# Performance work log

Measured on AMD Instinct MI355X. Metric: run time of the kernel, lower is better.

Reference implementation:

```python
import jax, jax.numpy as jnp
import numpy as np

S, B, D = 2048, 2, 4096
H, KVH, HD = 32, 8, 128          # n_heads_q, n_kv_heads, head_dim
NREP = H // KVH                  # GQA repeat factor
ROPE_BASE = 10000.0


def _rope(x, cos, sin):
    # x: [B, S, h, HD]; cos/sin: [S, HD//2]
    xr = x.reshape(x.shape[:-1] + (-1, 2))
    x0, x1 = xr[..., 0], xr[..., 1]
    c = cos[None, :, None, :]
    s = sin[None, :, None, :]
    out = jnp.stack([x0 * c - x1 * s, x0 * s + x1 * c], axis=-1)
    return out.reshape(x.shape)


def setup_inputs() -> dict:
    key = jax.random.key(0)
    k0, k1, k2, k3, k4 = jax.random.split(key, 5)
    x = jax.random.normal(k0, (S, B, D), jnp.float32)
    inv_freq = 1.0 / (ROPE_BASE ** (np.arange(0, HD, 2, dtype=np.float64) / HD))  # [HD//2]
    t = np.arange(S, dtype=np.float64)[:, None] * inv_freq[None, :]               # [S, HD//2]
    freqs_cos = jnp.asarray(np.cos(t), jnp.float32)
    freqs_sin = jnp.asarray(np.sin(t), jnp.float32)
    scale = 0.02
    wq = jax.random.normal(k1, (H * HD, D), jnp.float32) * scale
    wk = jax.random.normal(k2, (KVH * HD, D), jnp.float32) * scale
    wv = jax.random.normal(k3, (KVH * HD, D), jnp.float32) * scale
    wo = jax.random.normal(k4, (D, H * HD), jnp.float32) * scale
    return {"x": x, "start_pos": 0, "freqs_cos": freqs_cos, "freqs_sin": freqs_sin,
            "wq": wq, "wk": wk, "wv": wv, "wo": wo}


def reference(x, start_pos, freqs_cos, freqs_sin, wq, wk, wv, wo):
    seq_len, batch, _ = x.shape
    # QKV projections (torch Linear: y = x @ W^T), then [S,B,*] -> [B,S,h,HD]
    q = (x @ wq.T).transpose(1, 0, 2).reshape(batch, seq_len, H, HD)
    k = (x @ wk.T).transpose(1, 0, 2).reshape(batch, seq_len, KVH, HD)
    v = (x @ wv.T).transpose(1, 0, 2).reshape(batch, seq_len, KVH, HD)
    # RoPE on q and k
    q = _rope(q, freqs_cos, freqs_sin)
    k = _rope(k, freqs_cos, freqs_sin)
    # repeat_kv (GQA)
    k = jnp.repeat(k, NREP, axis=2)
    v = jnp.repeat(v, NREP, axis=2)
    # [B, H, S, HD]
    q = q.transpose(0, 2, 1, 3)
    k = k.transpose(0, 2, 1, 3)
    v = v.transpose(0, 2, 1, 3)
    # causal scaled dot-product attention (SDPA is_causal=True equivalent)
    scores = jnp.einsum('bhqd,bhkd->bhqk', q, k) / np.float32(np.sqrt(HD))
    causal = jnp.tril(jnp.ones((seq_len, seq_len), dtype=bool))
    scores = jnp.where(causal[None, None], scores, jnp.float32(-jnp.inf))
    probs = jax.nn.softmax(scores.astype(jnp.float32), axis=-1).astype(q.dtype)
    out = jnp.einsum('bhqk,bhkd->bhqd', probs, v)
    # [B,H,S,HD] -> [B,S,H*HD] -> [S,B,H*HD]
    out = out.transpose(0, 2, 1, 3).reshape(batch, seq_len, H * HD).transpose(1, 0, 2)
    return out @ wo.T
```

## Files before the change

### kernel.cpp

```cpp
#include <hip/hip_runtime.h>

typedef __attribute__((ext_vector_type(8))) short s16x8;
typedef __attribute__((ext_vector_type(8))) __bf16 bf16x8;
typedef __attribute__((ext_vector_type(4))) float f32x4;

#define S_LEN 2048
#define KDIM  4096
#define CSOFT 0.12751743f

__device__ __forceinline__ unsigned short f2bf(float f) {
  unsigned u = __builtin_bit_cast(unsigned, f);
  u += 0x7fffu + ((u >> 16) & 1u);
  return (unsigned short)(u >> 16);
}

__device__ __forceinline__ f32x4 mfma_bf16(s16x8 a, s16x8 b, f32x4 c) {
  return __builtin_amdgcn_mfma_f32_16x16x32_bf16(
      __builtin_bit_cast(bf16x8, a), __builtin_bit_cast(bf16x8, b), c, 0, 0, 0);
}

__device__ __forceinline__ void gload_lds16(const unsigned short* g, void* l) {
  __builtin_amdgcn_global_load_lds(
      (const __attribute__((address_space(1))) void*)g,
      (__attribute__((address_space(3))) void*)l, 16, 0, 0);
}

__device__ __forceinline__ void cvt8(const float* p, unsigned short* out) {
  f32x4 a = *(const f32x4*)(p);
  f32x4 b = *(const f32x4*)(p + 4);
  s16x8 v;
  v[0] = (short)f2bf(a[0]); v[1] = (short)f2bf(a[1]);
  v[2] = (short)f2bf(a[2]); v[3] = (short)f2bf(a[3]);
  v[4] = (short)f2bf(b[0]); v[5] = (short)f2bf(b[1]);
  v[6] = (short)f2bf(b[2]); v[7] = (short)f2bf(b[3]);
  *(s16x8*)(out) = v;
}

__global__ void cvt_bf16(const float* __restrict__ in,
                         unsigned short* __restrict__ out, int n8) {
  int i = blockIdx.x * 256 + threadIdx.x;
  if (i >= n8) return;
  cvt8(in + (size_t)i * 8, out + (size_t)i * 8);
}

__global__ void cvt_all(const float* __restrict__ x, const float* __restrict__ wq,
                        const float* __restrict__ wk, const float* __restrict__ wv,
                        const float* __restrict__ wo,
                        unsigned short* __restrict__ ox, unsigned short* __restrict__ oq,
                        unsigned short* __restrict__ ok, unsigned short* __restrict__ ov,
                        unsigned short* __restrict__ oo) {
  int blk = blockIdx.x;
  const float* src;
  unsigned short* dst;
  int i;
  if (blk < 8192) { src = x; dst = ox; i = blk; }
  else if (blk < 16384) { src = wq; dst = oq; i = blk - 8192; }
  else if (blk < 18432) { src = wk; dst = ok; i = blk - 16384; }
  else if (blk < 20480) { src = wv; dst = ov; i = blk - 18432; }
  else { src = wo; dst = oo; i = blk - 20480; }
  size_t idx = ((size_t)i * 256 + threadIdx.x) * 8;
  cvt8(src + idx, dst + idx);
}

template <int EPI>
__global__ __launch_bounds__(512, 1)
void gemm256(const unsigned short* __restrict__ A,
             const unsigned short* __restrict__ B,
             void* __restrict__ Out,
             const float* __restrict__ cosT,
             const float* __restrict__ sinT) {
  const int K = KDIM;
  __shared__ __align__(16) unsigned short As[2 * 2 * 8192];
  __shared__ __align__(16) unsigned short Bs[2 * 2 * 8192];

  const int tid = threadIdx.x;
  const int lane = tid & 63, wid = tid >> 6;
  const int l15 = lane & 15, l4 = lane >> 4;
  const int wr = wid >> 2, wc = wid & 3;

  int bid = blockIdx.x;
  {
  }
  const int xcd = bid & 7, ii = bid >> 3;
  const int rt = (xcd >> 1) * 4 + (ii >> 3);
  const int ct = (xcd & 1) * 8 + (ii & 7);
  const int row0 = rt * 256, col0 = ct * 256;

  const int ch0 = tid, ch1 = 512 + tid;
  const int sr0 = ch0 >> 3, u0 = (ch0 & 7) ^ (sr0 & 7);
  const int sr1 = ch1 >> 3, u1 = (ch1 & 7) ^ (sr1 & 7);
  const unsigned short* A0p = A + (size_t)(row0 + sr0) * K + u0 * 8;
  const unsigned short* A1p = A + (size_t)(row0 + sr1) * K + u1 * 8;
  const unsigned short* B0p = B + (size_t)(col0 + sr0) * K + u0 * 8;
  const unsigned short* B1p = B + (size_t)(col0 + sr1) * K + u1 * 8;

  const int rdo0 = l15 * 128 + ((l4 ^ (l15 & 7)) << 4);
  const int rdo1 = l15 * 128 + (((4 | l4) ^ (l15 & 7)) << 4);

  f32x4 acc[8][4];
#pragma unroll
  for (int m = 0; m < 8; m++)
#pragma unroll
    for (int n = 0; n < 4; n++) acc[m][n] = f32x4{0.f, 0.f, 0.f, 0.f};

  auto stageA = [&](int buf, int h, int kt) {
    char* d = (char*)As + buf * 32768 + h * 16384 + wid * 1024;
    size_t so = (size_t)h * 128 * K + kt;
    gload_lds16(A0p + so, d);
    gload_lds16(A1p + so, d + 8192);
  };
  auto stageB = [&](int buf, int h, int kt) {
    char* d = (char*)Bs + buf * 32768 + h * 16384 + wid * 1024;
    size_t so = (size_t)h * 128 * K + kt;
    gload_lds16(B0p + so, d);
    gload_lds16(B1p + so, d + 8192);
  };
  auto bar = [&]() { __builtin_amdgcn_s_barrier(); };
  auto quad = [&](const s16x8* ak0, const s16x8* ak1,
                  const s16x8* bk0, const s16x8* bk1, int mb, int nb) {
    __builtin_amdgcn_s_setprio(1);
#pragma unroll
    for (int mi = 0; mi < 4; mi++)
#pragma unroll
      for (int ni = 0; ni < 2; ni++) {
        acc[mb + mi][nb + ni] =
            mfma_bf16(ak0[mi], bk0[ni], acc[mb + mi][nb + ni]);
        acc[mb + mi][nb + ni] =
            mfma_bf16(ak1[mi], bk1[ni], acc[mb + mi][nb + ni]);
      }
    __builtin_amdgcn_s_setprio(0);
  };

  auto tile4 = [&](int buf, auto st1, auto st2, auto st3, auto st4,
                   int vmEnd) {
    const char* Ab = (const char*)As + buf * 32768 + wr * 16384;
    const char* Bb = (const char*)Bs + buf * 32768 + (wc >> 1) * 16384 +
                     (wc & 1) * 8192;
    s16x8 a0k0[4], a0k1[4], a1k0[4], a1k1[4];
    s16x8 b0k0[2], b0k1[2], b1k0[2], b1k1[2];

#pragma unroll
    for (int mi = 0; mi < 4; mi++) {
      a0k0[mi] = *(const s16x8*)(Ab + mi * 2048 + rdo0);
      a0k1[mi] = *(const s16x8*)(Ab + mi * 2048 + rdo1);
    }
#pragma unroll
    for (int ni = 0; ni < 2; ni++) {
      b0k0[ni] = *(const s16x8*)(Bb + ni * 2048 + rdo0);
      b0k1[ni] = *(const s16x8*)(Bb + ni * 2048 + rdo1);
    }
    st1();
    bar();
    quad(a0k0, a0k1, b0k0, b0k1, 0, 0);
    bar();

#pragma unroll
    for (int mi = 0; mi < 4; mi++) {
      a1k0[mi] = *(const s16x8*)(Ab + 8192 + mi * 2048 + rdo0);
      a1k1[mi] = *(const s16x8*)(Ab + 8192 + mi * 2048 + rdo1);
    }
#pragma unroll
    for (int ni = 0; ni < 2; ni++) {
      b1k0[ni] = *(const s16x8*)(Bb + 4096 + ni * 2048 + rdo0);
      b1k1[ni] = *(const s16x8*)(Bb + 4096 + ni * 2048 + rdo1);
    }
    st2();
    bar();
    quad(a1k0, a1k1, b0k0, b0k1, 4, 0);
    bar();

    st3();
    bar();
    quad(a0k0, a0k1, b1k0, b1k1, 0, 2);
    bar();

    st4();
    bar();
    quad(a1k0, a1k1, b1k0, b1k1, 4, 2);
    if (vmEnd == 4) {
      asm volatile("s_waitcnt vmcnt(4)" ::: "memory");
    } else if (vmEnd == 0) {
      asm volatile("s_waitcnt vmcnt(0)" ::: "memory");
    }
    bar();
  };
  auto nop = [&]() {};

  stageA(0, 0, 0);
  stageA(0, 1, 0);
  stageB(0, 0, 0);
  stageB(0, 1, 0);
  stageA(1, 0, 64);
  stageA(1, 1, 64);
  asm volatile("s_waitcnt vmcnt(4)" ::: "memory");
  bar();

  for (int j = 0; j < 31; j++) {
    const int k1 = (2 * j + 1) * 64, k2 = (2 * j + 2) * 64,
              k3 = (2 * j + 3) * 64;
    tile4(0, [&] { stageB(1, 0, k1); }, [&] { stageB(1, 1, k1); },
          [&] { stageA(0, 0, k2); }, [&] { stageA(0, 1, k2); }, 4);
    tile4(1, [&] { stageB(0, 0, k2); }, [&] { stageB(0, 1, k2); },
          [&] { stageA(1, 0, k3); }, [&] { stageA(1, 1, k3); }, 4);
  }
  {
    const int k1 = 63 * 64;
    tile4(0, [&] { stageB(1, 0, k1); }, [&] { stageB(1, 1, k1); }, nop, nop,
          0);
    tile4(1, nop, nop, nop, nop, -1);
  }

#pragma unroll
  for (int m = 0; m < 8; m++) {
#pragma unroll
    for (int n = 0; n < 4; n++) {
      f32x4 v = acc[m][n];
      int rowb = row0 + wr * 128 + m * 16 + l4 * 4;
      int col = col0 + wc * 64 + n * 16 + l15;
      if (EPI == 3) {
        float* o = (float*)Out;
#pragma unroll
        for (int r = 0; r < 4; r++) o[(size_t)(rowb + r) * 4096 + col] = v[r];
      } else {
        float vp[4];
#pragma unroll
        for (int r = 0; r < 4; r++) vp[r] = __shfl_xor(v[r], 1, 64);
        bool odd = lane & 1;
        int fi = (col & 127) >> 1;
#pragma unroll
        for (int r = 0; r < 4; r++) {
          int nn = rowb + r, s = nn >> 1;
          float c = cosT[s * 64 + fi], sn = sinT[s * 64 + fi];
          v[r] = odd ? (vp[r] * sn + v[r] * c) : (v[r] * c - vp[r] * sn);
        }
        unsigned short* o = (unsigned short*)Out;
        int hh = col >> 7, hd = col & 127;
#pragma unroll
        for (int r = 0; r < 4; r++) {
          int nn = rowb + r, s = nn >> 1, b = nn & 1;
          o[((size_t)(b * 32 + hh) * 2048 + s) * 128 + hd] = f2bf(v[r]);
        }
      }
    }
  }
}

template <int EPI, int N, bool B_FP32>
__global__ __launch_bounds__(256, 2)
void gemm_bt(const unsigned short* __restrict__ A,
             const float* __restrict__ Bw32,
             const unsigned short* __restrict__ Bw16,
             void* __restrict__ Out,
             const float* __restrict__ cosT,
             const float* __restrict__ sinT) {
  const int K = KDIM;
  const int tid = threadIdx.x;
  const int lane = tid & 63, wid = tid >> 6;
  const int l15 = lane & 15, l4 = lane >> 4;
  const int nct = N / 128;
  const int ct = blockIdx.x % nct, rt = blockIdx.x / nct;
  const int row0 = rt * 128, col0 = ct * 128;
  const int wr = wid >> 1, wc = wid & 1;

  __shared__ __align__(16) unsigned short As[128 * 32];
  __shared__ __align__(16) unsigned short Bs[128 * 32];

  f32x4 acc[4][4];
#pragma unroll
  for (int i = 0; i < 4; i++)
#pragma unroll
    for (int j = 0; j < 4; j++) acc[i][j] = f32x4{0.f, 0.f, 0.f, 0.f};

  for (int kt = 0; kt < K; kt += 32) {
#pragma unroll
    for (int i = 0; i < 2; i++) {
      int j = wid * 2 + i;
      int ch = j * 64 + lane;
      int r = ch >> 2, c = ch & 3;
      int sc = c ^ ((r >> 1) & 3);
      gload_lds16(A + (size_t)(row0 + r) * K + kt + sc * 8, (char*)As + j * 1024);
    }
    if (B_FP32) {
#pragma unroll
      for (int j = 0; j < 2; j++) {
        int ch = tid + 256 * j;
        int r = ch >> 2, c = ch & 3;
        const float* src = Bw32 + (size_t)(col0 + r) * K + kt + c * 8;
        f32x4 f0 = *(const f32x4*)(src);
        f32x4 f1 = *(const f32x4*)(src + 4);
        s16x8 v;
        v[0] = (short)f2bf(f0[0]); v[1] = (short)f2bf(f0[1]);
        v[2] = (short)f2bf(f0[2]); v[3] = (short)f2bf(f0[3]);
        v[4] = (short)f2bf(f1[0]); v[5] = (short)f2bf(f1[1]);
        v[6] = (short)f2bf(f1[2]); v[7] = (short)f2bf(f1[3]);
        int sw = c ^ ((r >> 1) & 3);
        *(s16x8*)((char*)Bs + r * 64 + sw * 16) = v;
      }
    } else {
#pragma unroll
      for (int i = 0; i < 2; i++) {
        int j = wid * 2 + i;
        int ch = j * 64 + lane;
        int r = ch >> 2, c = ch & 3;
        int sc = c ^ ((r >> 1) & 3);
        gload_lds16(Bw16 + (size_t)(col0 + r) * K + kt + sc * 8, (char*)Bs + j * 1024);
      }
    }
    __syncthreads();

    s16x8 af[4], bfr[4];
#pragma unroll
    for (int mi = 0; mi < 4; mi++) {
      int r = wr * 64 + mi * 16 + l15;
      int sw = l4 ^ ((r >> 1) & 3);
      af[mi] = *(const s16x8*)((char*)As + r * 64 + sw * 16);
    }
#pragma unroll
    for (int ni = 0; ni < 4; ni++) {
      int r = wc * 64 + ni * 16 + l15;
      int sw = l4 ^ ((r >> 1) & 3);
      bfr[ni] = *(const s16x8*)((char*)Bs + r * 64 + sw * 16);
    }
#pragma unroll
    for (int mi = 0; mi < 4; mi++)
#pragma unroll
      for (int ni = 0; ni < 4; ni++)
        acc[mi][ni] = mfma_bf16(af[mi], bfr[ni], acc[mi][ni]);
    __syncthreads();
  }

#pragma unroll
  for (int mi = 0; mi < 4; mi++) {
#pragma unroll
    for (int ni = 0; ni < 4; ni++) {
      f32x4 v = acc[mi][ni];
      int rowb = row0 + wr * 64 + mi * 16 + l4 * 4;
      int col = col0 + wc * 64 + ni * 16 + l15;
      if (EPI == 3) {
        float* o = (float*)Out;
#pragma unroll
        for (int r = 0; r < 4; r++) o[(size_t)(rowb + r) * 4096 + col] = v[r];
      } else {
        if (EPI != 2) {
          float vp[4];
#pragma unroll
          for (int r = 0; r < 4; r++) vp[r] = __shfl_xor(v[r], 1, 64);
          bool odd = lane & 1;
          int fi = (col & 127) >> 1;
#pragma unroll
          for (int r = 0; r < 4; r++) {
            int n = rowb + r, s = n >> 1;
            float c = cosT[s * 64 + fi], sn = sinT[s * 64 + fi];
            v[r] = odd ? (vp[r] * sn + v[r] * c) : (v[r] * c - vp[r] * sn);
          }
        }
        unsigned short* o = (unsigned short*)Out;
        int hh = col >> 7, hd = col & 127;
#pragma unroll
        for (int r = 0; r < 4; r++) {
          int n = rowb + r, s = n >> 1, b = n & 1;
          size_t idx;
          if (EPI == 0)      idx = ((size_t)(b * 32 + hh) * 2048 + s) * 128 + hd;
          else if (EPI == 1) idx = ((size_t)(b * 8 + hh) * 2048 + s) * 128 + hd;
          else               idx = ((size_t)(b * 8 + hh) * 128 + hd) * 2048 + s;
          o[idx] = f2bf(v[r]);
        }
      }
    }
  }
}

__global__ __launch_bounds__(256, 2)
void attn_fwd(const unsigned short* __restrict__ Qa,
              const unsigned short* __restrict__ Ka,
              const unsigned short* __restrict__ Vt,
              unsigned short* __restrict__ AO) {
  int bid = blockIdx.x;
  int xcd = bid & 7, slot = bid >> 3;
  int grp = xcd + 8 * (slot >> 5);
  int idx = slot & 31;
  int b = grp >> 3, kvh = grp & 7;
  int pid = idx & 7;
  int h = kvh * 4 + ((idx >> 3) & 3);
  int tid = threadIdx.x, lane = tid & 63, wid = tid >> 6;
  int l15 = lane & 15, l4 = lane >> 4;

  __shared__ __align__(16) unsigned short Ks[64 * 128];
  __shared__ __align__(16) unsigned short Vs[128 * 64];
  __shared__ __align__(16) unsigned short Ps[4][32 * 64];

  const unsigned short* Qp = Qa + ((size_t)(b * 32 + h) * 2048) * 128;
  const unsigned short* Kp = Ka + ((size_t)(b * 8 + kvh) * 2048) * 128;
  const unsigned short* Vp = Vt + ((size_t)(b * 8 + kvh) * 128) * 2048;

  for (int half = 0; half < 2; half++) {
    int qt = half == 0 ? (7 - pid) : (8 + pid);
    int q0 = qt * 128, qr0 = q0 + wid * 32;

    s16x8 qf[2][4];
#pragma unroll
    for (int mi = 0; mi < 2; mi++)
#pragma unroll
      for (int ks = 0; ks < 4; ks++)
        qf[mi][ks] = *(const s16x8*)(Qp + (size_t)(qr0 + mi * 16 + l15) * 128 +
                                     ks * 32 + l4 * 8);

    f32x4 o[2][8];
#pragma unroll
    for (int mi = 0; mi < 2; mi++)
#pragma unroll
      for (int nb = 0; nb < 8; nb++) o[mi][nb] = f32x4{0.f, 0.f, 0.f, 0.f};
    float m[2][4], lsum[2][4];
#pragma unroll
    for (int mi = 0; mi < 2; mi++)
#pragma unroll
      for (int pr = 0; pr < 4; pr++) { m[mi][pr] = -1e30f; lsum[mi][pr] = 0.f; }

    int nt = q0 / 64 + 2;
    for (int t = 0; t < nt; t++) {
      int s0 = t * 64;
      const unsigned short* ktp = Kp + (size_t)s0 * 128;
#pragma unroll
      for (int i = 0; i < 4; i++) {
        int j = wid * 4 + i;
        int ch = j * 64 + lane;
        {
          int r = ch >> 4, cl = ch & 15;
          int sc = (cl & 8) | ((cl ^ (r & 7)) & 7);
          gload_lds16(ktp + r * 128 + sc * 8, (char*)Ks + j * 1024);
        }
        {
          int r = ch >> 3, p = ch & 7;
          int sc = p ^ (r & 7);
          gload_lds16(Vp + (size_t)r * 2048 + s0 + sc * 8, (char*)Vs + j * 1024);
        }
      }
      __syncthreads();

      if (s0 <= qr0 + 31) {
        f32x4 sc[2][4];
#pragma unroll
        for (int mi = 0; mi < 2; mi++)
#pragma unroll
          for (int kb = 0; kb < 4; kb++) sc[mi][kb] = f32x4{0.f, 0.f, 0.f, 0.f};
        __builtin_amdgcn_s_setprio(1);
#pragma unroll
        for (int kb = 0; kb < 4; kb++) {
          int r = kb * 16 + l15;
#pragma unroll
          for (int ks = 0; ks < 4; ks++) {
            int c = ks * 4 + l4;
            int sw = (c & 8) | ((c ^ (r & 7)) & 7);
            s16x8 kf = *(const s16x8*)((char*)Ks + r * 256 + sw * 16);
            sc[0][kb] = mfma_bf16(qf[0][ks], kf, sc[0][kb]);
            sc[1][kb] = mfma_bf16(qf[1][ks], kf, sc[1][kb]);
          }
        }
        __builtin_amdgcn_s_setprio(0);
        bool needmask = (s0 + 63) > qr0;
#pragma unroll
        for (int mi = 0; mi < 2; mi++) {
          if (needmask) {
#pragma unroll
            for (int kb = 0; kb < 4; kb++) {
              int kg = s0 + kb * 16 + l15;
#pragma unroll
              for (int pr = 0; pr < 4; pr++) {
                int qg = qr0 + mi * 16 + l4 * 4 + pr;
                if (kg > qg) sc[mi][kb][pr] = -1e30f;
              }
            }
          }
          float rm[4];
#pragma unroll
          for (int pr = 0; pr < 4; pr++)
            rm[pr] = fmaxf(fmaxf(sc[mi][0][pr], sc[mi][1][pr]),
                           fmaxf(sc[mi][2][pr], sc[mi][3][pr]));
#pragma unroll
          for (int xm = 1; xm <= 8; xm <<= 1)
#pragma unroll
            for (int pr = 0; pr < 4; pr++)
              rm[pr] = fmaxf(rm[pr], __shfl_xor(rm[pr], xm, 64));
          bool grow = false;
#pragma unroll
          for (int pr = 0; pr < 4; pr++)
            grow = grow || ((rm[pr] - m[mi][pr]) * CSOFT > 8.f);
          if (__any(grow)) {
            float fac[4];
#pragma unroll
            for (int pr = 0; pr < 4; pr++) {
              float nm = fmaxf(m[mi][pr], rm[pr]);
              fac[pr] = __builtin_amdgcn_exp2f((m[mi][pr] - nm) * CSOFT);
              m[mi][pr] = nm;
              lsum[mi][pr] *= fac[pr];
            }
#pragma unroll
            for (int nb = 0; nb < 8; nb++)
#pragma unroll
              for (int pr = 0; pr < 4; pr++) o[mi][nb][pr] *= fac[pr];
          }
          float rs[4] = {0.f, 0.f, 0.f, 0.f};
#pragma unroll
          for (int kb = 0; kb < 4; kb++)
#pragma unroll
            for (int pr = 0; pr < 4; pr++) {
              float p = __builtin_amdgcn_exp2f((sc[mi][kb][pr] - m[mi][pr]) * CSOFT);
              sc[mi][kb][pr] = p;
              rs[pr] += p;
            }
#pragma unroll
          for (int xm = 1; xm <= 8; xm <<= 1)
#pragma unroll
            for (int pr = 0; pr < 4; pr++) rs[pr] += __shfl_xor(rs[pr], xm, 64);
#pragma unroll
          for (int pr = 0; pr < 4; pr++) lsum[mi][pr] += rs[pr];
          char* pb = (char*)(&Ps[wid][0]);
#pragma unroll
          for (int kb = 0; kb < 4; kb++) {
            int col = kb * 16 + l15;
#pragma unroll
            for (int pr = 0; pr < 4; pr++) {
              int row = mi * 16 + l4 * 4 + pr;
              *(unsigned short*)(pb + row * 128 + (((col >> 3) ^ (row & 7)) * 16) +
                                 (col & 7) * 2) = f2bf(sc[mi][kb][pr]);
            }
          }
        }
        char* pb = (char*)(&Ps[wid][0]);
        __builtin_amdgcn_s_setprio(1);
#pragma unroll
        for (int ks = 0; ks < 2; ks++) {
          s16x8 pa[2];
#pragma unroll
          for (int mi = 0; mi < 2; mi++) {
            int row = mi * 16 + l15;
            int c = ks * 4 + l4;
            pa[mi] = *(const s16x8*)(pb + row * 128 + ((c ^ (row & 7)) * 16));
          }
#pragma unroll
          for (int nb = 0; nb < 8; nb++) {
            int r = nb * 16 + l15;
            int c = ks * 4 + l4;
            s16x8 vf = *(const s16x8*)((char*)Vs + r * 128 + ((c ^ (r & 7)) * 16));
            o[0][nb] = mfma_bf16(pa[0], vf, o[0][nb]);
            o[1][nb] = mfma_bf16(pa[1], vf, o[1][nb]);
          }
        }
        __builtin_amdgcn_s_setprio(0);
      }
      __syncthreads();
    }

#pragma unroll
    for (int mi = 0; mi < 2; mi++) {
      float inv[4];
#pragma unroll
      for (int pr = 0; pr < 4; pr++) inv[pr] = 1.f / lsum[mi][pr];
#pragma unroll
      for (int nb = 0; nb < 8; nb++) {
        int col = h * 128 + nb * 16 + l15;
#pragma unroll
        for (int pr = 0; pr < 4; pr++) {
          int q = qr0 + mi * 16 + l4 * 4 + pr;
          AO[(size_t)(q * 2 + b) * 4096 + col] = f2bf(o[mi][nb][pr] * inv[pr]);
        }
      }
    }
  }
}

extern "C" void kernel_launch(void* const* d_in, const int* in_sizes, int n_in,
                              void* d_out, int out_size, void* d_ws, size_t ws_size,
                              hipStream_t stream) {
  const float* x = (const float*)d_in[0];
  const float* cosT = (const float*)d_in[2];
  const float* sinT = (const float*)d_in[3];
  const float* wq = (const float*)d_in[4];
  const float* wk = (const float*)d_in[5];
  const float* wv = (const float*)d_in[6];
  const float* wo = (const float*)d_in[7];
  float* out = (float*)d_out;

  char* ws = (char*)d_ws;
  unsigned short* xb = (unsigned short*)(ws);
  unsigned short* Qa = (unsigned short*)(ws + 33554432ull);
  unsigned short* Ka = (unsigned short*)(ws + 67108864ull);
  unsigned short* Vt = (unsigned short*)(ws + 75497472ull);
  unsigned short* AO = (unsigned short*)(ws + 83886080ull);
  unsigned short* wqb = (unsigned short*)(ws + 117440512ull);
  unsigned short* wkb = (unsigned short*)(ws + 150994944ull);
  unsigned short* wvb = (unsigned short*)(ws + 159383552ull);
  unsigned short* wob = (unsigned short*)(ws + 167772160ull);
  bool wcvt = ws_size >= 201326592ull;

  if (wcvt) {
    cvt_all<<<28672, 256, 0, stream>>>(x, wq, wk, wv, wo, xb, wqb, wkb, wvb, wob);
    gemm256<0><<<256, 512, 0, stream>>>(xb, wqb, Qa, cosT, sinT);
    gemm_bt<1, 1024, false><<<256, 256, 0, stream>>>(xb, nullptr, wkb, Ka, cosT, sinT);
    gemm_bt<2, 1024, false><<<256, 256, 0, stream>>>(xb, nullptr, wvb, Vt, cosT, sinT);
  } else {
    cvt_bf16<<<8192, 256, 0, stream>>>(x, xb, 2097152);
    gemm_bt<0, 4096, true><<<1024, 256, 0, stream>>>(xb, wq, nullptr, Qa, cosT, sinT);
    gemm_bt<1, 1024, true><<<256, 256, 0, stream>>>(xb, wk, nullptr, Ka, cosT, sinT);
    gemm_bt<2, 1024, true><<<256, 256, 0, stream>>>(xb, wv, nullptr, Vt, cosT, sinT);
  }
  attn_fwd<<<512, 256, 0, stream>>>(Qa, Ka, Vt, AO);
  if (wcvt) {
    gemm256<3><<<256, 512, 0, stream>>>(AO, wob, out, cosT, sinT);
  } else {
    gemm_bt<3, 4096, true><<<1024, 256, 0, stream>>>(AO, wo, nullptr, out, cosT, sinT);
  }
}
```

Before: 619.4 us.

## Merge K and V projection GEMMs into one launch and trim gemm256 barriers

Replaces the two separate K and V projection launches with a single gemm_kv kernel of 512 blocks. The first half of the blocks computes K with the RoPE epilogue and the second half computes V with a transposed store, which fills the GPU in one launch instead of two half-sized ones. The gemm256 inner tile is also restructured from four barrier-separated stages to three: the B1 fragment loads move later, the two A stage loads are merged, and one barrier pair between the last two MFMA quads is removed. The new gemm_kv uses a simple single-buffered 32-wide K loop with full syncs, which may be less efficient than the previous gemm_bt pipeline.

```diff
diff --git a/kernel.cpp b/kernel.cpp
--- a/kernel.cpp
+++ b/kernel.cpp
@@ -79,8 +79,6 @@
   const int wr = wid >> 2, wc = wid & 3;
 
   int bid = blockIdx.x;
-  {
-  }
   const int xcd = bid & 7, ii = bid >> 3;
   const int rt = (xcd >> 1) * 4 + (ii >> 3);
   const int ct = (xcd & 1) * 8 + (ii & 7);
@@ -131,8 +129,7 @@
     __builtin_amdgcn_s_setprio(0);
   };
 
-  auto tile4 = [&](int buf, auto st1, auto st2, auto st3, auto st4,
-                   int vmEnd) {
+  auto tile3 = [&](int buf, auto st1, auto st2, auto st3, int vmEnd) {
     const char* Ab = (const char*)As + buf * 32768 + wr * 16384;
     const char* Bb = (const char*)Bs + buf * 32768 + (wc >> 1) * 16384 +
                      (wc & 1) * 8192;
@@ -159,23 +156,19 @@
       a1k0[mi] = *(const s16x8*)(Ab + 8192 + mi * 2048 + rdo0);
       a1k1[mi] = *(const s16x8*)(Ab + 8192 + mi * 2048 + rdo1);
     }
-#pragma unroll
-    for (int ni = 0; ni < 2; ni++) {
-      b1k0[ni] = *(const s16x8*)(Bb + 4096 + ni * 2048 + rdo0);
-      b1k1[ni] = *(const s16x8*)(Bb + 4096 + ni * 2048 + rdo1);
-    }
     st2();
     bar();
     quad(a1k0, a1k1, b0k0, b0k1, 4, 0);
     bar();
 
+#pragma unroll
+    for (int ni = 0; ni < 2; ni++) {
+      b1k0[ni] = *(const s16x8*)(Bb + 4096 + ni * 2048 + rdo0);
+      b1k1[ni] = *(const s16x8*)(Bb + 4096 + ni * 2048 + rdo1);
+    }
     st3();
     bar();
     quad(a0k0, a0k1, b1k0, b1k1, 0, 2);
-    bar();
-
-    st4();
-    bar();
     quad(a1k0, a1k1, b1k0, b1k1, 4, 2);
     if (vmEnd == 4) {
       asm volatile("s_waitcnt vmcnt(4)" ::: "memory");
@@ -198,16 +191,15 @@
   for (int j = 0; j < 31; j++) {
     const int k1 = (2 * j + 1) * 64, k2 = (2 * j + 2) * 64,
               k3 = (2 * j + 3) * 64;
-    tile4(0, [&] { stageB(1, 0, k1); }, [&] { stageB(1, 1, k1); },
-          [&] { stageA(0, 0, k2); }, [&] { stageA(0, 1, k2); }, 4);
-    tile4(1, [&] { stageB(0, 0, k2); }, [&] { stageB(0, 1, k2); },
-          [&] { stageA(1, 0, k3); }, [&] { stageA(1, 1, k3); }, 4);
+    tile3(0, [&] { stageB(1, 0, k1); }, [&] { stageB(1, 1, k1); },
+          [&] { stageA(0, 0, k2); stageA(0, 1, k2); }, 4);
+    tile3(1, [&] { stageB(0, 0, k2); }, [&] { stageB(0, 1, k2); },
+          [&] { stageA(1, 0, k3); stageA(1, 1, k3); }, 4);
   }
   {
     const int k1 = 63 * 64;
-    tile4(0, [&] { stageB(1, 0, k1); }, [&] { stageB(1, 1, k1); }, nop, nop,
-          0);
-    tile4(1, nop, nop, nop, nop, -1);
+    tile3(0, [&] { stageB(1, 0, k1); }, [&] { stageB(1, 1, k1); }, nop, 0);
+    tile3(1, nop, nop, nop, -1);
   }
 
 #pragma unroll
@@ -239,6 +231,104 @@
         for (int r = 0; r < 4; r++) {
           int nn = rowb + r, s = nn >> 1, b = nn & 1;
           o[((size_t)(b * 32 + hh) * 2048 + s) * 128 + hd] = f2bf(v[r]);
+        }
+      }
+    }
+  }
+}
+
+__global__ __launch_bounds__(256, 2)
+void gemm_kv(const unsigned short* __restrict__ A,
+             const unsigned short* __restrict__ Bk,
+             const unsigned short* __restrict__ Bv,
+             unsigned short* __restrict__ OutK,
+             unsigned short* __restrict__ OutV,
+             const float* __restrict__ cosT,
+             const float* __restrict__ sinT) {
+  const int K = KDIM;
+  const int tid = threadIdx.x;
+  const int lane = tid & 63, wid = tid >> 6;
+  const int l15 = lane & 15, l4 = lane >> 4;
+  const bool isV = blockIdx.x >= 256;
+  const int lb = blockIdx.x & 255;
+  const int ct = lb & 7, rt = lb >> 3;
+  const int row0 = rt * 128, col0 = ct * 128;
+  const int wr = wid >> 1, wc = wid & 1;
+  const unsigned short* Bw = isV ? Bv : Bk;
+
+  __shared__ __align__(16) unsigned short As[128 * 32];
+  __shared__ __align__(16) unsigned short Bs[128 * 32];
+
+  f32x4 acc[4][4];
+#pragma unroll
+  for (int i = 0; i < 4; i++)
+#pragma unroll
+    for (int j = 0; j < 4; j++) acc[i][j] = f32x4{0.f, 0.f, 0.f, 0.f};
+
+  for (int kt = 0; kt < K; kt += 32) {
+#pragma unroll
+    for (int i = 0; i < 2; i++) {
+      int j = wid * 2 + i;
+      int ch = j * 64 + lane;
+      int r = ch >> 2, c = ch & 3;
+      int sc = c ^ ((r >> 1) & 3);
+      gload_lds16(A + (size_t)(row0 + r) * K + kt + sc * 8, (char*)As + j * 1024);
+      gload_lds16(Bw + (size_t)(col0 + r) * K + kt + sc * 8, (char*)Bs + j * 1024);
+    }
+    __syncthreads();
+
+    s16x8 af[4], bfr[4];
+#pragma unroll
+    for (int mi = 0; mi < 4; mi++) {
+      int r = wr * 64 + mi * 16 + l15;
+      int sw = l4 ^ ((r >> 1) & 3);
+      af[mi] = *(const s16x8*)((char*)As + r * 64 + sw * 16);
+    }
+#pragma unroll
+    for (int ni = 0; ni < 4; ni++) {
+      int r = wc * 64 + ni * 16 + l15;
+      int sw = l4 ^ ((r >> 1) & 3);
+      bfr[ni] = *(const s16x8*)((char*)Bs + r * 64 + sw * 16);
+    }
+#pragma unroll
+    for (int mi = 0; mi < 4; mi++)
+#pragma unroll
+      for (int ni = 0; ni < 4; ni++)
+        acc[mi][ni] = mfma_bf16(af[mi], bfr[ni], acc[mi][ni]);
+    __syncthreads();
+  }
+
+#pragma unroll
+  for (int mi = 0; mi < 4; mi++) {
+#pragma unroll
+    for (int ni = 0; ni < 4; ni++) {
+      f32x4 v = acc[mi][ni];
+      int rowb = row0 + wr * 64 + mi * 16 + l4 * 4;
+      int col = col0 + wc * 64 + ni * 16 + l15;
+      if (!isV) {
+        float vp[4];
+#pragma unroll
+        for (int r = 0; r < 4; r++) vp[r] = __shfl_xor(v[r], 1, 64);
+        bool odd = lane & 1;
+        int fi = (col & 127) >> 1;
+#pragma unroll
+        for (int r = 0; r < 4; r++) {
+          int n = rowb + r, s = n >> 1;
+          float c = cosT[s * 64 + fi], sn = sinT[s * 64 + fi];
+          v[r] = odd ? (vp[r] * sn + v[r] * c) : (v[r] * c - vp[r] * sn);
+        }
+        int hh = col >> 7, hd = col & 127;
+#pragma unroll
+        for (int r = 0; r < 4; r++) {
+          int n = rowb + r, s = n >> 1, b = n & 1;
+          OutK[((size_t)(b * 8 + hh) * 2048 + s) * 128 + hd] = f2bf(v[r]);
+        }
+      } else {
+        int hh = col >> 7, hd = col & 127;
+#pragma unroll
+        for (int r = 0; r < 4; r++) {
+          int n = rowb + r, s = n >> 1, b = n & 1;
+          OutV[((size_t)(b * 8 + hh) * 128 + hd) * 2048 + s] = f2bf(v[r]);
         }
       }
     }
@@ -596,8 +686,7 @@
   if (wcvt) {
     cvt_all<<<28672, 256, 0, stream>>>(x, wq, wk, wv, wo, xb, wqb, wkb, wvb, wob);
     gemm256<0><<<256, 512, 0, stream>>>(xb, wqb, Qa, cosT, sinT);
-    gemm_bt<1, 1024, false><<<256, 256, 0, stream>>>(xb, nullptr, wkb, Ka, cosT, sinT);
-    gemm_bt<2, 1024, false><<<256, 256, 0, stream>>>(xb, nullptr, wvb, Vt, cosT, sinT);
+    gemm_kv<<<512, 256, 0, stream>>>(xb, wkb, wvb, Ka, Vt, cosT, sinT);
   } else {
     cvt_bf16<<<8192, 256, 0, stream>>>(x, xb, 2097152);
     gemm_bt<0, 4096, true><<<1024, 256, 0, stream>>>(xb, wq, nullptr, Qa, cosT, sinT);
```

Result: faster. 547.0 us (-11.7%).
